# Kernel tuning notes

Hardware: AMD Instinct MI355X
Metric: run time of the kernel (lower is better)

## Reference

```python
import jax, jax.numpy as jnp
import numpy as np

NQ = 200000; K = 4; M = 64; KEY = 64; V = 128; E = 64; B = 512; S = 200

def setup_inputs() -> dict:
    key = jax.random.key(0)
    ks = jax.random.split(key, 16)
    return {
        'q_embed_table': jax.random.normal(ks[0], (NQ + 1, E), jnp.float32) * 0.1,
        'alpha_mean': jax.random.normal(ks[1], (NQ,), jnp.float32) * 0.2,
        'beta_base': jax.random.normal(ks[2], (NQ,), jnp.float32) * 0.5,
        'beta_gaps': jax.random.uniform(ks[3], (NQ, K - 2), jnp.float32) * 0.5 + 0.25,
        'ability_means': jax.random.normal(ks[4], (M, V), jnp.float32) * 0.1,
        'ability_log_vars': jnp.zeros((M, V), jnp.float32),
        'memory_keys': jax.random.normal(ks[5], (M, KEY), jnp.float32),
        'q_to_key_w': jax.random.normal(ks[6], (E, KEY), jnp.float32) / np.sqrt(E),
        'q_to_key_b': jnp.zeros((KEY,), jnp.float32),
        'qa_embed_w': jax.random.normal(ks[7], (2, E), jnp.float32),
        'qa_embed_b': jnp.zeros((E,), jnp.float32),
        'qa_to_ev_w': jax.random.normal(ks[8], (E, V), jnp.float32) / np.sqrt(E),
        'qa_to_ev_b': jnp.zeros((V,), jnp.float32),
        'questions': jax.random.randint(ks[9], (B, S), 0, NQ),
        'responses': jax.random.randint(ks[10], (B, S), 0, K),
    }


def reference(q_embed_table, alpha_mean, beta_base, beta_gaps, ability_means,
              ability_log_vars, memory_keys, q_to_key_w, q_to_key_b,
              qa_embed_w, qa_embed_b, qa_to_ev_w, qa_to_ev_b,
              questions, responses):
    nQ = alpha_mean.shape[0]
    Kc = beta_gaps.shape[1] + 2  # n_categories

    # --- gather question-specific IRT params (irregular gather) ---
    alphas = jnp.exp(alpha_mean[questions])                      # [B,S]
    base = beta_base[questions]                                  # [B,S]
    gaps = jax.nn.softplus(beta_gaps[questions])                 # [B,S,K-2]
    # cumulative thresholds: beta_0 = base, beta_k = beta_{k-1} + gap_{k-1}
    betas = jnp.cumsum(jnp.concatenate([base[..., None], gaps], axis=-1), axis=-1)  # [B,S,K-1]

    # --- attention over memory slots ---
    q_emb = q_embed_table[questions]                             # [B,S,E]
    queries = q_emb @ q_to_key_w + q_to_key_b                    # [B,S,KEY]
    attn = jax.nn.softmax(jnp.einsum('bsk,mk->bsm', queries, memory_keys), axis=-1)  # [B,S,M]

    # --- evidence embedding from (question, response) ---
    qn = questions.astype(jnp.float32) / nQ
    rn = responses.astype(jnp.float32) / (Kc - 1)
    qa = jnp.stack([qn, rn], axis=-1) @ qa_embed_w + qa_embed_b  # [B,S,E]
    evidence = jnp.tanh(qa) @ qa_to_ev_w + qa_to_ev_b            # [B,S,V]

    # --- sequential memory read + per-slot Bayesian scatter update ---
    def step(carry, inp):
        means, log_vars = carry                                  # [M,V] each
        attn_t, ev_t = inp                                       # [B,M], [B,V]
        theta = jnp.mean(attn_t @ means, axis=-1)                # bayesian_read -> [B]
        # precision-weighted update of every slot (evidence_precision = 1)
        w = jnp.mean(attn_t, axis=0)                             # [M] update weights
        ev_mean = jnp.mean(ev_t, axis=0)                         # [V]
        prior_prec = jnp.exp(-log_vars)
        post_prec = prior_prec + w[:, None]
        post_mean = (prior_prec * means + ev_mean[None, :] * w[:, None]) / post_prec
        # torch updates under no_grad -> stop_gradient
        new_means = jax.lax.stop_gradient(post_mean)
        new_lv = jax.lax.stop_gradient(-jnp.log(post_prec))
        return (new_means, new_lv), theta

    (_, _), thetas = jax.lax.scan(
        step, (ability_means, ability_log_vars),
        (attn.transpose(1, 0, 2), evidence.transpose(1, 0, 2)))
    thetas = thetas.T                                            # [B,S]

    # --- GPCM category probabilities ---
    z = alphas[..., None] * (thetas[..., None] - betas)          # [B,S,K-1]
    cum = jnp.concatenate([jnp.zeros_like(z[..., :1]), jnp.cumsum(z, axis=-1)], axis=-1)  # [B,S,K]
    probs = jax.nn.softmax(cum, axis=-1)
    return probs
```

## Files before the change

### kernel.cpp

```cpp
#include <hip/hip_runtime.h>
#include <math.h>

#define M_SLOTS 64
#define E_DIM   64
#define KEY_DIM 64
#define V_DIM   128
#define K_CAT   4
#define S_LEN   200

typedef __attribute__((ext_vector_type(8)))  short short8;
typedef __attribute__((ext_vector_type(16))) float f32x16;

#define OFF_CT     0
#define OFF_BM     2048
#define OFF_WBAR   2112
#define OFF_BBAR   2176
#define OFF_RM0    2240
#define OFF_P0     2304
#define OFF_WSUM   2368
#define OFF_EMSUM  (OFF_WSUM + S_LEN*M_SLOTS)

#define PRE_CT_END   4096
#define PRE_BM_END   4160
#define PRE_WBAR_END 4224
#define PRE_BBAR     4224
#define PRE_RM_BEG   4225
#define PRE_RM_END   4289
#define PRE_Z_BEG    4289
#define PRE_Z_END    (4289 + S_LEN*M_SLOTS + S_LEN)

__device__ __forceinline__ unsigned pk2rne(float lo, float hi) {
    unsigned ul = __float_as_uint(lo); ul += 0x7fffu + ((ul >> 16) & 1u);
    unsigned uh = __float_as_uint(hi); uh += 0x7fffu + ((uh >> 16) & 1u);
    return __builtin_amdgcn_perm(uh, ul, 0x07060302u);
}
__device__ __forceinline__ unsigned short bf16rne(float f) {
    unsigned u = __float_as_uint(f);
    return (unsigned short)((u + 0x7fffu + ((u >> 16) & 1u)) >> 16);
}
__device__ __forceinline__ short8 as_s8(uint4 u) { return __builtin_bit_cast(short8, u); }

__device__ __forceinline__ void gpcm_store(float th, int q,
                                           const float* __restrict__ alpha_mean,
                                           const float* __restrict__ beta_base,
                                           const float* __restrict__ beta_gaps,
                                           float* __restrict__ out, size_t idx) {
    float a  = __expf(alpha_mean[q]);
    float b0 = beta_base[q];
    float2 g = *reinterpret_cast<const float2*>(&beta_gaps[q * (K_CAT - 2)]);
    float g0 = log1pf(__expf(g.x));
    float g1 = log1pf(__expf(g.y));
    float be1 = b0 + g0;
    float be2 = be1 + g1;
    float z0 = a * (th - b0);
    float z1 = a * (th - be1);
    float z2 = a * (th - be2);
    float c1 = z0, c2 = z0 + z1, c3 = z0 + z1 + z2;
    float cm = fmaxf(fmaxf(0.f, c1), fmaxf(c2, c3));
    float e0 = __expf(0.f - cm), e1 = __expf(c1 - cm), e2 = __expf(c2 - cm), e3 = __expf(c3 - cm);
    float si = __fdividef(1.0f, e0 + e1 + e2 + e3);
    float4 o4 = make_float4(e0 * si, e1 * si, e2 * si, e3 * si);
    *reinterpret_cast<float4*>(&out[idx * K_CAT]) = o4;
}

__device__ __forceinline__ void mfma_logits(
    const float* __restrict__ qrow, const unsigned short* __restrict__ ct,
    const float* __restrict__ bm, int h, int p, f32x16 acc[2])
{
    float4 qf[8];
    #pragma unroll
    for (int s = 0; s < 4; ++s) {
        const float4* src = (const float4*)(qrow + s * 16 + h * 8);
        qf[2 * s]     = src[0];
        qf[2 * s + 1] = src[1];
    }
    uint4 af[8];
    #pragma unroll
    for (int mt = 0; mt < 2; ++mt)
        #pragma unroll
        for (int s = 0; s < 4; ++s)
            af[mt * 4 + s] = *(const uint4*)(ct + (p + 32 * mt) * E_DIM + s * 16 + h * 8);
    #pragma unroll
    for (int mt = 0; mt < 2; ++mt)
        #pragma unroll
        for (int g = 0; g < 4; ++g) {
            float4 v = *(const float4*)(bm + 8 * g + 4 * h + 32 * mt);
            acc[mt][4 * g + 0] = v.x; acc[mt][4 * g + 1] = v.y;
            acc[mt][4 * g + 2] = v.z; acc[mt][4 * g + 3] = v.w;
        }
    #pragma unroll
    for (int s = 0; s < 4; ++s) {
        uint4 bf;
        bf.x = pk2rne(qf[2 * s].x,     qf[2 * s].y);
        bf.y = pk2rne(qf[2 * s].z,     qf[2 * s].w);
        bf.z = pk2rne(qf[2 * s + 1].x, qf[2 * s + 1].y);
        bf.w = pk2rne(qf[2 * s + 1].z, qf[2 * s + 1].w);
        short8 bfr = as_s8(bf);
        acc[0] = __builtin_amdgcn_mfma_f32_32x32x16_bf16(as_s8(af[s]),     bfr, acc[0], 0, 0, 0);
        acc[1] = __builtin_amdgcn_mfma_f32_32x32x16_bf16(as_s8(af[4 + s]), bfr, acc[1], 0, 0, 0);
    }
}

__global__ void k_pre(const float* __restrict__ q2k_w, const float* __restrict__ q2k_b,
                      const float* __restrict__ mkeys,
                      const float* __restrict__ ev_w, const float* __restrict__ ev_b,
                      const float* __restrict__ means, const float* __restrict__ logvars,
                      float* __restrict__ ws) {
    int gid = blockIdx.x * blockDim.x + threadIdx.x;
    if (gid < PRE_CT_END) {
        int e = gid >> 6, m = gid & 63;
        float s = 0.f;
        #pragma unroll
        for (int k = 0; k < KEY_DIM; ++k) s = fmaf(q2k_w[e * KEY_DIM + k], mkeys[m * KEY_DIM + k], s);
        ((unsigned short*)ws)[m * E_DIM + e] = bf16rne(s);
    } else if (gid < PRE_BM_END) {
        int m = gid - PRE_CT_END;
        float s = 0.f;
        #pragma unroll
        for (int k = 0; k < KEY_DIM; ++k) s = fmaf(q2k_b[k], mkeys[m * KEY_DIM + k], s);
        ws[OFF_BM + m] = s;
    } else if (gid < PRE_WBAR_END) {
        int e = gid - PRE_BM_END;
        float s = 0.f;
        for (int v = 0; v < V_DIM; ++v) s += ev_w[e * V_DIM + v];
        ws[OFF_WBAR + e] = s * (1.0f / V_DIM);
    } else if (gid == PRE_BBAR) {
        float s = 0.f;
        for (int v = 0; v < V_DIM; ++v) s += ev_b[v];
        ws[OFF_BBAR] = s * (1.0f / V_DIM);
    } else if (gid >= PRE_RM_BEG && gid < PRE_RM_END) {
        int m = gid - PRE_RM_BEG;
        const float4* mr = (const float4*)(means + (size_t)m * V_DIM);
        float s = 0.f;
        #pragma unroll
        for (int i = 0; i < V_DIM / 4; ++i) { float4 v = mr[i]; s += (v.x + v.y) + (v.z + v.w); }
        ws[OFF_RM0 + m] = s * (1.0f / V_DIM);
        ws[OFF_P0 + m]  = __expf(-logvars[(size_t)m * V_DIM]);
    } else if (gid >= PRE_Z_BEG && gid < PRE_Z_END) {
        ws[OFF_WSUM + (gid - PRE_Z_BEG)] = 0.f;
    }
}

__global__ __launch_bounds__(256, 3) void k_attn(
    const float* __restrict__ qtab, const int* __restrict__ qs, const int* __restrict__ rs,
    const float* __restrict__ ws_ro,
    const float* __restrict__ qa_w, const float* __restrict__ qa_b,
    float* __restrict__ wsum, float* __restrict__ emsum,
    int B, float invNQ)
{
    __shared__ float4 lsEv[64];
    const int tid = threadIdx.x, wv = tid >> 6, lane = tid & 63;
    const int h = lane >> 5, p = lane & 31;
    const int t = blockIdx.x;
    const int b = blockIdx.y * 128 + wv * 32 + p;

    const int q = qs[(size_t)b * S_LEN + t];
    const int r = rs[(size_t)b * S_LEN + t];

    if (tid < 64) lsEv[tid] = make_float4(qa_w[tid], qa_w[E_DIM + tid], qa_b[tid],
                                          ws_ro[OFF_WBAR + tid]);
    const float bb = ws_ro[OFF_BBAR];

    f32x16 acc[2];
    mfma_logits(qtab + (size_t)q * E_DIM, (const unsigned short*)ws_ro,
                ws_ro + OFF_BM, h, p, acc);

    float av[32];
    float ssum = 0.f;
    #pragma unroll
    for (int j = 0; j < 16; ++j) { av[j]      = __expf(acc[0][j]); ssum += av[j]; }
    #pragma unroll
    for (int j = 0; j < 16; ++j) { av[16 + j] = __expf(acc[1][j]); ssum += av[16 + j]; }
    ssum += __shfl_xor(ssum, 32);
    const float inv = __fdividef(1.0f, ssum);

    #pragma unroll
    for (int j = 0; j < 32; ++j) av[j] *= inv;
    #pragma unroll
    for (int step = 0; step < 5; ++step) {
        const int sh = 1 << step;
        #pragma unroll
        for (int j = 0; j < (32 >> step) / 2; ++j) {
            float p0 = av[2 * j]     + __shfl_xor(av[2 * j], sh);
            float p1 = av[2 * j + 1] + __shfl_xor(av[2 * j + 1], sh);
            av[j] = (lane & sh) ? p1 : p0;
        }
    }
    {
        const int jj = lane & 31;
        const int m = (jj & 3) + 8 * ((jj >> 2) & 3) + 4 * h + 32 * (jj >> 4);
        atomicAdd(&wsum[t * M_SLOTS + m], av[0]);
    }

    __syncthreads();

    float qn = (float)q * invNQ;
    float rn = (float)r * (1.0f / (K_CAT - 1));
    float evm = 0.f;
    #pragma unroll 8
    for (int e = 0; e < 32; ++e) {
        float4 pv = lsEv[h * 32 + e];
        float qa = fmaf(qn, pv.x, fmaf(rn, pv.y, pv.z));
        float ez = __expf(2.0f * qa);
        evm = fmaf(__fdividef(ez - 1.0f, ez + 1.0f), pv.w, evm);
    }
    evm += __shfl_xor(evm, 32);
    evm += bb;
    #pragma unroll
    for (int o = 16; o; o >>= 1) evm += __shfl_xor(evm, o);
    if (!lane) atomicAdd(&emsum[t], evm);
}

__global__ __launch_bounds__(256, 3) void k_out(
    const float* __restrict__ qtab, const int* __restrict__ qs,
    const float* __restrict__ ws_ro,
    const float* __restrict__ alpha_mean, const float* __restrict__ beta_base,
    const float* __restrict__ beta_gaps, float* __restrict__ out, int B, float invB)
{
    __shared__ float lsW[4][M_SLOTS], lsN[4][M_SLOTS];
    __shared__ float lsRmP[M_SLOTS];
    const int tid = threadIdx.x, wv = tid >> 6, lane = tid & 63;
    const int h = lane >> 5, p = lane & 31;
    const int t = blockIdx.x;
    const int b = blockIdx.y * 128 + wv * 32 + p;

    const int q = qs[(size_t)b * S_LEN + t];

    {
        const float* wsum  = ws_ro + OFF_WSUM;
        const float* emsum = ws_ro + OFF_EMSUM;
        const int seg = (t + 3) >> 2;
        const int s0 = wv * seg, s1 = min(s0 + seg, t);
        float pw = 0.f, pn = 0.f;
        for (int s = s0; s < s1; ++s) {
            float w = wsum[s * M_SLOTS + lane];
            pw += w;
            pn = fmaf(emsum[s], w, pn);
        }
        lsW[wv][lane] = pw; lsN[wv][lane] = pn;
    }
    __syncthreads();
    if (tid < 64) {
        const int m = tid;
        float sw = lsW[0][m] + lsW[1][m] + lsW[2][m] + lsW[3][m];
        float sn = lsN[0][m] + lsN[1][m] + lsN[2][m] + lsN[3][m];
        float den = ws_ro[OFF_P0 + m] + sw * invB;
        float num = ws_ro[OFF_P0 + m] * ws_ro[OFF_RM0 + m] + sn * (invB * invB);
        const int idx = ((m >> 2) & 1) * 32 + ((m >> 5) & 1) * 16 + (m & 3) + 4 * ((m >> 3) & 3);
        lsRmP[idx] = num / den;
    }
    __syncthreads();

    f32x16 acc[2];
    mfma_logits(qtab + (size_t)q * E_DIM, (const unsigned short*)ws_ro,
                ws_ro + OFF_BM, h, p, acc);

    float ssum = 0.f, th = 0.f;
    const float* rmh = lsRmP + h * 32;
    #pragma unroll
    for (int j = 0; j < 16; ++j) {
        float e = __expf(acc[0][j]);
        ssum += e;
        th = fmaf(e, rmh[j], th);
    }
    #pragma unroll
    for (int j = 0; j < 16; ++j) {
        float e = __expf(acc[1][j]);
        ssum += e;
        th = fmaf(e, rmh[16 + j], th);
    }
    ssum += __shfl_xor(ssum, 32);
    th   += __shfl_xor(th, 32);
    th = __fdividef(th, ssum);

    if (!h) gpcm_store(th, q, alpha_mean, beta_base, beta_gaps, out, (size_t)b * S_LEN + t);
}

extern "C" void kernel_launch(void* const* d_in, const int* in_sizes, int n_in,
                              void* d_out, int out_size, void* d_ws, size_t ws_size,
                              hipStream_t stream) {
    const float* qtab       = (const float*)d_in[0];
    const float* alpha_mean = (const float*)d_in[1];
    const float* beta_base  = (const float*)d_in[2];
    const float* beta_gaps  = (const float*)d_in[3];
    const float* ab_means   = (const float*)d_in[4];
    const float* ab_logvars = (const float*)d_in[5];
    const float* mkeys      = (const float*)d_in[6];
    const float* q2k_w      = (const float*)d_in[7];
    const float* q2k_b      = (const float*)d_in[8];
    const float* qa_w       = (const float*)d_in[9];
    const float* qa_b       = (const float*)d_in[10];
    const float* ev_w       = (const float*)d_in[11];
    const float* ev_b       = (const float*)d_in[12];
    const int*   qs         = (const int*)d_in[13];
    const int*   rs         = (const int*)d_in[14];
    float* out = (float*)d_out;
    float* ws  = (float*)d_ws;

    const int NQ = in_sizes[1];
    const int S  = S_LEN;
    const int B  = in_sizes[13] / S;

    float* wsum  = ws + OFF_WSUM;
    float* emsum = ws + OFF_EMSUM;

    k_pre<<<(PRE_Z_END + 255) / 256, 256, 0, stream>>>(
        q2k_w, q2k_b, mkeys, ev_w, ev_b, ab_means, ab_logvars, ws);

    dim3 g(S, B / 128);
    k_attn<<<g, 256, 0, stream>>>(qtab, qs, rs, ws, qa_w, qa_b,
                                  wsum, emsum, B, 1.0f / (float)NQ);

    k_out<<<g, 256, 0, stream>>>(qtab, qs, ws, alpha_mean, beta_base,
                                 beta_gaps, out, B, 1.0f / (float)B);
}
```

Before: 49.37 us.

## Switch attention logits to 16x16x32 bf16 MFMA with 16 rows per wave

Replaces the 32x32x16 MFMA logits tile (32 batch rows per wave, two 32-slot tiles) with 16x16x32 MFMA tiles covering 16 batch rows per wave and four 16-slot tiles. The grid doubles along the batch dimension, the reductions and shuffles are remapped to the new lane layout, and launch bounds go from 3 to 4 waves per SIMD. The goal is smaller accumulators, more resident waves and more blocks for latency hiding. The cost is twice as many blocks, each reloading the shared weight tiles and running more atomics per time step.

After: 56.76 us. +15.0%, slower.

```diff
diff --git a/kernel.cpp b/kernel.cpp
--- a/kernel.cpp
+++ b/kernel.cpp
@@ -8,8 +8,8 @@
 #define K_CAT   4
 #define S_LEN   200
 
-typedef __attribute__((ext_vector_type(8)))  short short8;
-typedef __attribute__((ext_vector_type(16))) float f32x16;
+typedef __attribute__((ext_vector_type(8))) short short8;
+typedef __attribute__((ext_vector_type(4))) float f32x4;
 
 #define OFF_CT     0
 #define OFF_BM     2048
@@ -63,42 +63,37 @@
     *reinterpret_cast<float4*>(&out[idx * K_CAT]) = o4;
 }
 
-__device__ __forceinline__ void mfma_logits(
+__device__ __forceinline__ void mfma_logits16(
     const float* __restrict__ qrow, const unsigned short* __restrict__ ct,
-    const float* __restrict__ bm, int h, int p, f32x16 acc[2])
+    const float* __restrict__ bm, int kg, int p16, f32x4 acc[4])
 {
-    float4 qf[8];
-    #pragma unroll
-    for (int s = 0; s < 4; ++s) {
-        const float4* src = (const float4*)(qrow + s * 16 + h * 8);
-        qf[2 * s]     = src[0];
-        qf[2 * s + 1] = src[1];
-    }
-    uint4 af[8];
-    #pragma unroll
-    for (int mt = 0; mt < 2; ++mt)
-        #pragma unroll
-        for (int s = 0; s < 4; ++s)
-            af[mt * 4 + s] = *(const uint4*)(ct + (p + 32 * mt) * E_DIM + s * 16 + h * 8);
-    #pragma unroll
-    for (int mt = 0; mt < 2; ++mt)
-        #pragma unroll
-        for (int g = 0; g < 4; ++g) {
-            float4 v = *(const float4*)(bm + 8 * g + 4 * h + 32 * mt);
-            acc[mt][4 * g + 0] = v.x; acc[mt][4 * g + 1] = v.y;
-            acc[mt][4 * g + 2] = v.z; acc[mt][4 * g + 3] = v.w;
-        }
-    #pragma unroll
-    for (int s = 0; s < 4; ++s) {
-        uint4 bf;
-        bf.x = pk2rne(qf[2 * s].x,     qf[2 * s].y);
-        bf.y = pk2rne(qf[2 * s].z,     qf[2 * s].w);
-        bf.z = pk2rne(qf[2 * s + 1].x, qf[2 * s + 1].y);
-        bf.w = pk2rne(qf[2 * s + 1].z, qf[2 * s + 1].w);
-        short8 bfr = as_s8(bf);
-        acc[0] = __builtin_amdgcn_mfma_f32_32x32x16_bf16(as_s8(af[s]),     bfr, acc[0], 0, 0, 0);
-        acc[1] = __builtin_amdgcn_mfma_f32_32x32x16_bf16(as_s8(af[4 + s]), bfr, acc[1], 0, 0, 0);
-    }
+    float4 qa = *(const float4*)(qrow + kg * 8);
+    float4 qb = *(const float4*)(qrow + kg * 8 + 4);
+    float4 qc = *(const float4*)(qrow + 32 + kg * 8);
+    float4 qd = *(const float4*)(qrow + 32 + kg * 8 + 4);
+    uint4 af[4][2];
+    #pragma unroll
+    for (int mt = 0; mt < 4; ++mt)
+        #pragma unroll
+        for (int c = 0; c < 2; ++c)
+            af[mt][c] = *(const uint4*)(ct + (mt * 16 + p16) * E_DIM + c * 32 + kg * 8);
+    #pragma unroll
+    for (int mt = 0; mt < 4; ++mt) {
+        float4 v = *(const float4*)(bm + mt * 16 + kg * 4);
+        acc[mt][0] = v.x; acc[mt][1] = v.y; acc[mt][2] = v.z; acc[mt][3] = v.w;
+    }
+    uint4 b0u, b1u;
+    b0u.x = pk2rne(qa.x, qa.y); b0u.y = pk2rne(qa.z, qa.w);
+    b0u.z = pk2rne(qb.x, qb.y); b0u.w = pk2rne(qb.z, qb.w);
+    b1u.x = pk2rne(qc.x, qc.y); b1u.y = pk2rne(qc.z, qc.w);
+    b1u.z = pk2rne(qd.x, qd.y); b1u.w = pk2rne(qd.z, qd.w);
+    short8 b0 = as_s8(b0u), b1 = as_s8(b1u);
+    #pragma unroll
+    for (int mt = 0; mt < 4; ++mt)
+        acc[mt] = __builtin_amdgcn_mfma_f32_16x16x32_bf16(as_s8(af[mt][0]), b0, acc[mt], 0, 0, 0);
+    #pragma unroll
+    for (int mt = 0; mt < 4; ++mt)
+        acc[mt] = __builtin_amdgcn_mfma_f32_16x16x32_bf16(as_s8(af[mt][1]), b1, acc[mt], 0, 0, 0);
 }
 
 __global__ void k_pre(const float* __restrict__ q2k_w, const float* __restrict__ q2k_b,
@@ -141,7 +136,7 @@
     }
 }
 
-__global__ __launch_bounds__(256, 3) void k_attn(
+__global__ __launch_bounds__(256, 4) void k_attn(
     const float* __restrict__ qtab, const int* __restrict__ qs, const int* __restrict__ rs,
     const float* __restrict__ ws_ro,
     const float* __restrict__ qa_w, const float* __restrict__ qa_b,
@@ -150,9 +145,9 @@
 {
     __shared__ float4 lsEv[64];
     const int tid = threadIdx.x, wv = tid >> 6, lane = tid & 63;
-    const int h = lane >> 5, p = lane & 31;
+    const int p16 = lane & 15, kg = lane >> 4;
     const int t = blockIdx.x;
-    const int b = blockIdx.y * 128 + wv * 32 + p;
+    const int b = blockIdx.y * 64 + wv * 16 + p16;
 
     const int q = qs[(size_t)b * S_LEN + t];
     const int r = rs[(size_t)b * S_LEN + t];
@@ -161,34 +156,40 @@
                                           ws_ro[OFF_WBAR + tid]);
     const float bb = ws_ro[OFF_BBAR];
 
-    f32x16 acc[2];
-    mfma_logits(qtab + (size_t)q * E_DIM, (const unsigned short*)ws_ro,
-                ws_ro + OFF_BM, h, p, acc);
-
-    float av[32];
+    f32x4 acc[4];
+    mfma_logits16(qtab + (size_t)q * E_DIM, (const unsigned short*)ws_ro,
+                  ws_ro + OFF_BM, kg, p16, acc);
+
+    float ex[16];
     float ssum = 0.f;
     #pragma unroll
-    for (int j = 0; j < 16; ++j) { av[j]      = __expf(acc[0][j]); ssum += av[j]; }
-    #pragma unroll
-    for (int j = 0; j < 16; ++j) { av[16 + j] = __expf(acc[1][j]); ssum += av[16 + j]; }
+    for (int mt = 0; mt < 4; ++mt)
+        #pragma unroll
+        for (int rg = 0; rg < 4; ++rg) {
+            float e = __expf(acc[mt][rg]);
+            ex[mt * 4 + rg] = e;
+            ssum += e;
+        }
+    ssum += __shfl_xor(ssum, 16);
     ssum += __shfl_xor(ssum, 32);
     const float inv = __fdividef(1.0f, ssum);
 
-    #pragma unroll
-    for (int j = 0; j < 32; ++j) av[j] *= inv;
-    #pragma unroll
-    for (int step = 0; step < 5; ++step) {
+    float av[16];
+    #pragma unroll
+    for (int j = 0; j < 16; ++j) av[j] = ex[j] * inv;
+    #pragma unroll
+    for (int step = 0; step < 4; ++step) {
         const int sh = 1 << step;
         #pragma unroll
-        for (int j = 0; j < (32 >> step) / 2; ++j) {
+        for (int j = 0; j < (16 >> step) / 2; ++j) {
             float p0 = av[2 * j]     + __shfl_xor(av[2 * j], sh);
             float p1 = av[2 * j + 1] + __shfl_xor(av[2 * j + 1], sh);
             av[j] = (lane & sh) ? p1 : p0;
         }
     }
     {
-        const int jj = lane & 31;
-        const int m = (jj & 3) + 8 * ((jj >> 2) & 3) + 4 * h + 32 * (jj >> 4);
+        const int jj = lane & 15;
+        const int m = (jj >> 2) * 16 + kg * 4 + (jj & 3);
         atomicAdd(&wsum[t * M_SLOTS + m], av[0]);
     }
 
@@ -197,32 +198,33 @@
     float qn = (float)q * invNQ;
     float rn = (float)r * (1.0f / (K_CAT - 1));
     float evm = 0.f;
-    #pragma unroll 8
-    for (int e = 0; e < 32; ++e) {
-        float4 pv = lsEv[h * 32 + e];
+    #pragma unroll
+    for (int i = 0; i < 16; ++i) {
+        float4 pv = lsEv[kg * 16 + i];
         float qa = fmaf(qn, pv.x, fmaf(rn, pv.y, pv.z));
         float ez = __expf(2.0f * qa);
         evm = fmaf(__fdividef(ez - 1.0f, ez + 1.0f), pv.w, evm);
     }
+    evm += __shfl_xor(evm, 16);
     evm += __shfl_xor(evm, 32);
     evm += bb;
     #pragma unroll
-    for (int o = 16; o; o >>= 1) evm += __shfl_xor(evm, o);
+    for (int o = 8; o; o >>= 1) evm += __shfl_xor(evm, o);
     if (!lane) atomicAdd(&emsum[t], evm);
 }
 
-__global__ __launch_bounds__(256, 3) void k_out(
+__global__ __launch_bounds__(256, 4) void k_out(
     const float* __restrict__ qtab, const int* __restrict__ qs,
     const float* __restrict__ ws_ro,
     const float* __restrict__ alpha_mean, const float* __restrict__ beta_base,
     const float* __restrict__ beta_gaps, float* __restrict__ out, int B, float invB)
 {
     __shared__ float lsW[4][M_SLOTS], lsN[4][M_SLOTS];
-    __shared__ float lsRmP[M_SLOTS];
+    __shared__ float lsRm[M_SLOTS];
     const int tid = threadIdx.x, wv = tid >> 6, lane = tid & 63;
-    const int h = lane >> 5, p = lane & 31;
+    const int p16 = lane & 15, kg = lane >> 4;
     const int t = blockIdx.x;
-    const int b = blockIdx.y * 128 + wv * 32 + p;
+    const int b = blockIdx.y * 64 + wv * 16 + p16;
 
     const int q = qs[(size_t)b * S_LEN + t];
 
@@ -246,34 +248,30 @@
         float sn = lsN[0][m] + lsN[1][m] + lsN[2][m] + lsN[3][m];
         float den = ws_ro[OFF_P0 + m] + sw * invB;
         float num = ws_ro[OFF_P0 + m] * ws_ro[OFF_RM0 + m] + sn * (invB * invB);
-        const int idx = ((m >> 2) & 1) * 32 + ((m >> 5) & 1) * 16 + (m & 3) + 4 * ((m >> 3) & 3);
-        lsRmP[idx] = num / den;
+        lsRm[m] = num / den;
     }
     __syncthreads();
 
-    f32x16 acc[2];
-    mfma_logits(qtab + (size_t)q * E_DIM, (const unsigned short*)ws_ro,
-                ws_ro + OFF_BM, h, p, acc);
+    f32x4 acc[4];
+    mfma_logits16(qtab + (size_t)q * E_DIM, (const unsigned short*)ws_ro,
+                  ws_ro + OFF_BM, kg, p16, acc);
 
     float ssum = 0.f, th = 0.f;
-    const float* rmh = lsRmP + h * 32;
-    #pragma unroll
-    for (int j = 0; j < 16; ++j) {
-        float e = __expf(acc[0][j]);
-        ssum += e;
-        th = fmaf(e, rmh[j], th);
-    }
-    #pragma unroll
-    for (int j = 0; j < 16; ++j) {
-        float e = __expf(acc[1][j]);
-        ssum += e;
-        th = fmaf(e, rmh[16 + j], th);
-    }
+    #pragma unroll
+    for (int mt = 0; mt < 4; ++mt)
+        #pragma unroll
+        for (int rg = 0; rg < 4; ++rg) {
+            float e = __expf(acc[mt][rg]);
+            ssum += e;
+            th = fmaf(e, lsRm[mt * 16 + kg * 4 + rg], th);
+        }
+    ssum += __shfl_xor(ssum, 16);
     ssum += __shfl_xor(ssum, 32);
+    th   += __shfl_xor(th, 16);
     th   += __shfl_xor(th, 32);
     th = __fdividef(th, ssum);
 
-    if (!h) gpcm_store(th, q, alpha_mean, beta_base, beta_gaps, out, (size_t)b * S_LEN + t);
+    if (kg == 0) gpcm_store(th, q, alpha_mean, beta_base, beta_gaps, out, (size_t)b * S_LEN + t);
 }
 
 extern "C" void kernel_launch(void* const* d_in, const int* in_sizes, int n_in,
@@ -307,7 +305,7 @@
     k_pre<<<(PRE_Z_END + 255) / 256, 256, 0, stream>>>(
         q2k_w, q2k_b, mkeys, ev_w, ev_b, ab_means, ab_logvars, ws);
 
-    dim3 g(S, B / 128);
+    dim3 g(S, B / 64);
     k_attn<<<g, 256, 0, stream>>>(qtab, qs, rs, ws, qa_w, qa_b,
                                   wsum, emsum, B, 1.0f / (float)NQ);
 
```

## Transpose question/response indices and compute per-step ability means in separate kernel

Applied to the files above, without the earlier changes.

k_pre now also transposes the question and response index arrays into time-major order in the workspace, so k_attn and k_out read indices with coalesced accesses instead of strided ones. The prefix-sum reduction of slot weights and evidence, which every k_out block recomputed redundantly, moves into a new k_rm kernel that runs once per time step and writes the posterior means to the workspace. This removes redundant per-block work from k_out but adds one kernel launch and a serial transpose pass over the indices inside k_pre.

Result: slower. 58.98 us (+19.5%).

```diff
diff --git a/kernel.cpp b/kernel.cpp
--- a/kernel.cpp
+++ b/kernel.cpp
@@ -19,6 +19,9 @@
 #define OFF_P0     2304
 #define OFF_WSUM   2368
 #define OFF_EMSUM  (OFF_WSUM + S_LEN*M_SLOTS)
+#define OFF_QST    15424
+#define OFF_RST    (OFF_QST + S_LEN*512)
+#define OFF_RM     (OFF_RST + S_LEN*512)
 
 #define PRE_CT_END   4096
 #define PRE_BM_END   4160
@@ -28,6 +31,7 @@
 #define PRE_RM_END   4289
 #define PRE_Z_BEG    4289
 #define PRE_Z_END    (4289 + S_LEN*M_SLOTS + S_LEN)
+#define PRE_T_BEG    PRE_Z_END
 
 __device__ __forceinline__ unsigned pk2rne(float lo, float hi) {
     unsigned ul = __float_as_uint(lo); ul += 0x7fffu + ((ul >> 16) & 1u);
@@ -105,7 +109,8 @@
                       const float* __restrict__ mkeys,
                       const float* __restrict__ ev_w, const float* __restrict__ ev_b,
                       const float* __restrict__ means, const float* __restrict__ logvars,
-                      float* __restrict__ ws) {
+                      const int* __restrict__ qs, const int* __restrict__ rs,
+                      float* __restrict__ ws, int B) {
     int gid = blockIdx.x * blockDim.x + threadIdx.x;
     if (gid < PRE_CT_END) {
         int e = gid >> 6, m = gid & 63;
@@ -138,12 +143,22 @@
         ws[OFF_P0 + m]  = __expf(-logvars[(size_t)m * V_DIM]);
     } else if (gid >= PRE_Z_BEG && gid < PRE_Z_END) {
         ws[OFF_WSUM + (gid - PRE_Z_BEG)] = 0.f;
+    } else {
+        int i = gid - PRE_T_BEG;
+        const int SB = S_LEN * B;
+        if (i < SB) {
+            int t = i / B, b = i - t * B;
+            ((int*)(ws + OFF_QST))[i] = qs[(size_t)b * S_LEN + t];
+        } else if (i < 2 * SB) {
+            int j = i - SB;
+            int t = j / B, b = j - t * B;
+            ((int*)(ws + OFF_RST))[j] = rs[(size_t)b * S_LEN + t];
+        }
     }
 }
 
 __global__ __launch_bounds__(256, 3) void k_attn(
-    const float* __restrict__ qtab, const int* __restrict__ qs, const int* __restrict__ rs,
-    const float* __restrict__ ws_ro,
+    const float* __restrict__ qtab, const float* __restrict__ ws_ro,
     const float* __restrict__ qa_w, const float* __restrict__ qa_b,
     float* __restrict__ wsum, float* __restrict__ emsum,
     int B, float invNQ)
@@ -154,8 +169,8 @@
     const int t = blockIdx.x;
     const int b = blockIdx.y * 128 + wv * 32 + p;
 
-    const int q = qs[(size_t)b * S_LEN + t];
-    const int r = rs[(size_t)b * S_LEN + t];
+    const int q = ((const int*)(ws_ro + OFF_QST))[t * B + b];
+    const int r = ((const int*)(ws_ro + OFF_RST))[t * B + b];
 
     if (tid < 64) lsEv[tid] = make_float4(qa_w[tid], qa_w[E_DIM + tid], qa_b[tid],
                                           ws_ro[OFF_WBAR + tid]);
@@ -211,44 +226,48 @@
     if (!lane) atomicAdd(&emsum[t], evm);
 }
 
+__global__ __launch_bounds__(64) void k_rm(
+    const float* __restrict__ ws_ro, float* __restrict__ rm, float invB)
+{
+    const int t = blockIdx.x, m = threadIdx.x;
+    const float* wsum  = ws_ro + OFF_WSUM;
+    const float* emsum = ws_ro + OFF_EMSUM;
+    float den = ws_ro[OFF_P0 + m];
+    float num = den * ws_ro[OFF_RM0 + m];
+    int s = 0;
+    for (; s + 4 <= t; s += 4) {
+        float w0 = wsum[(s + 0) * M_SLOTS + m] * invB;
+        float w1 = wsum[(s + 1) * M_SLOTS + m] * invB;
+        float w2 = wsum[(s + 2) * M_SLOTS + m] * invB;
+        float w3 = wsum[(s + 3) * M_SLOTS + m] * invB;
+        num = fmaf(emsum[s + 0] * invB, w0, num); den += w0;
+        num = fmaf(emsum[s + 1] * invB, w1, num); den += w1;
+        num = fmaf(emsum[s + 2] * invB, w2, num); den += w2;
+        num = fmaf(emsum[s + 3] * invB, w3, num); den += w3;
+    }
+    for (; s < t; ++s) {
+        float w = wsum[s * M_SLOTS + m] * invB;
+        num = fmaf(emsum[s] * invB, w, num);
+        den += w;
+    }
+    const int idx = ((m >> 2) & 1) * 32 + ((m >> 5) & 1) * 16 + (m & 3) + 4 * ((m >> 3) & 3);
+    rm[t * M_SLOTS + idx] = num / den;
+}
+
 __global__ __launch_bounds__(256, 3) void k_out(
-    const float* __restrict__ qtab, const int* __restrict__ qs,
-    const float* __restrict__ ws_ro,
+    const float* __restrict__ qtab, const float* __restrict__ ws_ro,
+    const float* __restrict__ rm,
     const float* __restrict__ alpha_mean, const float* __restrict__ beta_base,
-    const float* __restrict__ beta_gaps, float* __restrict__ out, int B, float invB)
+    const float* __restrict__ beta_gaps, float* __restrict__ out, int B)
 {
-    __shared__ float lsW[4][M_SLOTS], lsN[4][M_SLOTS];
-    __shared__ float lsRmP[M_SLOTS];
+    __shared__ float lsRm[M_SLOTS];
     const int tid = threadIdx.x, wv = tid >> 6, lane = tid & 63;
     const int h = lane >> 5, p = lane & 31;
     const int t = blockIdx.x;
     const int b = blockIdx.y * 128 + wv * 32 + p;
 
-    const int q = qs[(size_t)b * S_LEN + t];
-
-    {
-        const float* wsum  = ws_ro + OFF_WSUM;
-        const float* emsum = ws_ro + OFF_EMSUM;
-        const int seg = (t + 3) >> 2;
-        const int s0 = wv * seg, s1 = min(s0 + seg, t);
-        float pw = 0.f, pn = 0.f;
-        for (int s = s0; s < s1; ++s) {
-            float w = wsum[s * M_SLOTS + lane];
-            pw += w;
-            pn = fmaf(emsum[s], w, pn);
-        }
-        lsW[wv][lane] = pw; lsN[wv][lane] = pn;
-    }
-    __syncthreads();
-    if (tid < 64) {
-        const int m = tid;
-        float sw = lsW[0][m] + lsW[1][m] + lsW[2][m] + lsW[3][m];
-        float sn = lsN[0][m] + lsN[1][m] + lsN[2][m] + lsN[3][m];
-        float den = ws_ro[OFF_P0 + m] + sw * invB;
-        float num = ws_ro[OFF_P0 + m] * ws_ro[OFF_RM0 + m] + sn * (invB * invB);
-        const int idx = ((m >> 2) & 1) * 32 + ((m >> 5) & 1) * 16 + (m & 3) + 4 * ((m >> 3) & 3);
-        lsRmP[idx] = num / den;
-    }
+    const int q = ((const int*)(ws_ro + OFF_QST))[t * B + b];
+    if (tid < 64) lsRm[tid] = rm[t * M_SLOTS + tid];
     __syncthreads();
 
     f32x16 acc[2];
@@ -256,7 +275,7 @@
                 ws_ro + OFF_BM, h, p, acc);
 
     float ssum = 0.f, th = 0.f;
-    const float* rmh = lsRmP + h * 32;
+    const float* rmh = lsRm + h * 32;
     #pragma unroll
     for (int j = 0; j < 16; ++j) {
         float e = __expf(acc[0][j]);
@@ -303,14 +322,17 @@
 
     float* wsum  = ws + OFF_WSUM;
     float* emsum = ws + OFF_EMSUM;
-
-    k_pre<<<(PRE_Z_END + 255) / 256, 256, 0, stream>>>(
-        q2k_w, q2k_b, mkeys, ev_w, ev_b, ab_means, ab_logvars, ws);
+    float* rm    = ws + OFF_RM;
+
+    const int pre_items = PRE_T_BEG + 2 * S * B;
+    k_pre<<<(pre_items + 255) / 256, 256, 0, stream>>>(
+        q2k_w, q2k_b, mkeys, ev_w, ev_b, ab_means, ab_logvars, qs, rs, ws, B);
 
     dim3 g(S, B / 128);
-    k_attn<<<g, 256, 0, stream>>>(qtab, qs, rs, ws, qa_w, qa_b,
-                                  wsum, emsum, B, 1.0f / (float)NQ);
-
-    k_out<<<g, 256, 0, stream>>>(qtab, qs, ws, alpha_mean, beta_base,
-                                 beta_gaps, out, B, 1.0f / (float)B);
-}
+    k_attn<<<g, 256, 0, stream>>>(qtab, ws, qa_w, qa_b, wsum, emsum, B, 1.0f / (float)NQ);
+
+    k_rm<<<S, 64, 0, stream>>>(ws, rm, 1.0f / (float)B);
+
+    k_out<<<g, 256, 0, stream>>>(qtab, ws, rm, alpha_mean, beta_base,
+                                 beta_gaps, out, B);
+}
```

## Fuse precompute kernel into attention kernels and replace atomics with per-block partials

Applied to the files above, without the earlier changes.

Removes the k_pre launch. Every block of k_attn and k_out now rebuilds the bf16 key-projection matrix with MFMA into swizzled LDS and computes the bias and mean terms locally. Global atomicAdds into wsum/emsum are replaced by an LDS reduction and plain per-block partial stores, which also removes the need to zero the workspace. k_out sums the four partials. The aim is to save a launch, the zeroing pass and atomic contention, at the cost of redundant per-block recompute and more LDS use.

After: 61.34 us. 24.2% more time.

```diff
diff --git a/kernel.cpp b/kernel.cpp
--- a/kernel.cpp
+++ b/kernel.cpp
@@ -11,23 +11,8 @@
 typedef __attribute__((ext_vector_type(8)))  short short8;
 typedef __attribute__((ext_vector_type(16))) float f32x16;
 
-#define OFF_CT     0
-#define OFF_BM     2048
-#define OFF_WBAR   2112
-#define OFF_BBAR   2176
-#define OFF_RM0    2240
-#define OFF_P0     2304
-#define OFF_WSUM   2368
-#define OFF_EMSUM  (OFF_WSUM + S_LEN*M_SLOTS)
-
-#define PRE_CT_END   4096
-#define PRE_BM_END   4160
-#define PRE_WBAR_END 4224
-#define PRE_BBAR     4224
-#define PRE_RM_BEG   4225
-#define PRE_RM_END   4289
-#define PRE_Z_BEG    4289
-#define PRE_Z_END    (4289 + S_LEN*M_SLOTS + S_LEN)
+#define OFF_WSUMP  0
+#define OFF_EMSUMP (S_LEN * 4 * M_SLOTS)
 
 __device__ __forceinline__ unsigned pk2rne(float lo, float hi) {
     unsigned ul = __float_as_uint(lo); ul += 0x7fffu + ((ul >> 16) & 1u);
@@ -63,31 +48,48 @@
     *reinterpret_cast<float4*>(&out[idx * K_CAT]) = o4;
 }
 
-__device__ __forceinline__ void mfma_logits(
-    const float* __restrict__ qrow, const unsigned short* __restrict__ ct,
-    const float* __restrict__ bm, int h, int p, f32x16 acc[2])
+__device__ __forceinline__ void ct_build(const float* __restrict__ q2k_w,
+                                         const float* __restrict__ mkeys,
+                                         unsigned short* ctL, int wv, int h, int p) {
+    const int m0 = (wv & 1) * 32, e0 = (wv >> 1) * 32;
+    f32x16 d;
+    #pragma unroll
+    for (int i = 0; i < 16; ++i) d[i] = 0.f;
+    #pragma unroll
+    for (int s = 0; s < 4; ++s) {
+        const float* ar = mkeys + (m0 + p) * KEY_DIM + s * 16 + h * 8;
+        const float* br = q2k_w + (e0 + p) * KEY_DIM + s * 16 + h * 8;
+        float4 a0 = *(const float4*)ar, a1 = *(const float4*)(ar + 4);
+        float4 b0 = *(const float4*)br, b1 = *(const float4*)(br + 4);
+        uint4 au, bu;
+        au.x = pk2rne(a0.x, a0.y); au.y = pk2rne(a0.z, a0.w);
+        au.z = pk2rne(a1.x, a1.y); au.w = pk2rne(a1.z, a1.w);
+        bu.x = pk2rne(b0.x, b0.y); bu.y = pk2rne(b0.z, b0.w);
+        bu.z = pk2rne(b1.x, b1.y); bu.w = pk2rne(b1.z, b1.w);
+        d = __builtin_amdgcn_mfma_f32_32x32x16_bf16(as_s8(au), as_s8(bu), d, 0, 0, 0);
+    }
+    #pragma unroll
+    for (int j = 0; j < 16; ++j) {
+        int row = (j & 3) + 8 * ((j >> 2) & 3) + 4 * h;
+        int m = m0 + row, e = e0 + p;
+        int off = m * 128 + (((e * 2)) ^ ((m & 7) << 4));
+        *(unsigned short*)((char*)ctL + off) = bf16rne(d[j]);
+    }
+}
+
+__device__ __forceinline__ void mfma_logits_lds(
+    const float4 qf[8], const unsigned short* ctL, const float* bmL,
+    int h, int p, f32x16 acc[2])
 {
-    float4 qf[8];
-    #pragma unroll
-    for (int s = 0; s < 4; ++s) {
-        const float4* src = (const float4*)(qrow + s * 16 + h * 8);
-        qf[2 * s]     = src[0];
-        qf[2 * s + 1] = src[1];
-    }
-    uint4 af[8];
     #pragma unroll
     for (int mt = 0; mt < 2; ++mt)
         #pragma unroll
-        for (int s = 0; s < 4; ++s)
-            af[mt * 4 + s] = *(const uint4*)(ct + (p + 32 * mt) * E_DIM + s * 16 + h * 8);
-    #pragma unroll
-    for (int mt = 0; mt < 2; ++mt)
-        #pragma unroll
         for (int g = 0; g < 4; ++g) {
-            float4 v = *(const float4*)(bm + 8 * g + 4 * h + 32 * mt);
+            float4 v = *(const float4*)(bmL + 8 * g + 4 * h + 32 * mt);
             acc[mt][4 * g + 0] = v.x; acc[mt][4 * g + 1] = v.y;
             acc[mt][4 * g + 2] = v.z; acc[mt][4 * g + 3] = v.w;
         }
+    const int sw = (p & 7) << 4;
     #pragma unroll
     for (int s = 0; s < 4; ++s) {
         uint4 bf;
@@ -96,74 +98,75 @@
         bf.z = pk2rne(qf[2 * s + 1].x, qf[2 * s + 1].y);
         bf.w = pk2rne(qf[2 * s + 1].z, qf[2 * s + 1].w);
         short8 bfr = as_s8(bf);
-        acc[0] = __builtin_amdgcn_mfma_f32_32x32x16_bf16(as_s8(af[s]),     bfr, acc[0], 0, 0, 0);
-        acc[1] = __builtin_amdgcn_mfma_f32_32x32x16_bf16(as_s8(af[4 + s]), bfr, acc[1], 0, 0, 0);
-    }
-}
-
-__global__ void k_pre(const float* __restrict__ q2k_w, const float* __restrict__ q2k_b,
-                      const float* __restrict__ mkeys,
-                      const float* __restrict__ ev_w, const float* __restrict__ ev_b,
-                      const float* __restrict__ means, const float* __restrict__ logvars,
-                      float* __restrict__ ws) {
-    int gid = blockIdx.x * blockDim.x + threadIdx.x;
-    if (gid < PRE_CT_END) {
-        int e = gid >> 6, m = gid & 63;
-        float s = 0.f;
-        #pragma unroll
-        for (int k = 0; k < KEY_DIM; ++k) s = fmaf(q2k_w[e * KEY_DIM + k], mkeys[m * KEY_DIM + k], s);
-        ((unsigned short*)ws)[m * E_DIM + e] = bf16rne(s);
-    } else if (gid < PRE_BM_END) {
-        int m = gid - PRE_CT_END;
-        float s = 0.f;
-        #pragma unroll
-        for (int k = 0; k < KEY_DIM; ++k) s = fmaf(q2k_b[k], mkeys[m * KEY_DIM + k], s);
-        ws[OFF_BM + m] = s;
-    } else if (gid < PRE_WBAR_END) {
-        int e = gid - PRE_BM_END;
-        float s = 0.f;
-        for (int v = 0; v < V_DIM; ++v) s += ev_w[e * V_DIM + v];
-        ws[OFF_WBAR + e] = s * (1.0f / V_DIM);
-    } else if (gid == PRE_BBAR) {
-        float s = 0.f;
-        for (int v = 0; v < V_DIM; ++v) s += ev_b[v];
-        ws[OFF_BBAR] = s * (1.0f / V_DIM);
-    } else if (gid >= PRE_RM_BEG && gid < PRE_RM_END) {
-        int m = gid - PRE_RM_BEG;
-        const float4* mr = (const float4*)(means + (size_t)m * V_DIM);
-        float s = 0.f;
-        #pragma unroll
-        for (int i = 0; i < V_DIM / 4; ++i) { float4 v = mr[i]; s += (v.x + v.y) + (v.z + v.w); }
-        ws[OFF_RM0 + m] = s * (1.0f / V_DIM);
-        ws[OFF_P0 + m]  = __expf(-logvars[(size_t)m * V_DIM]);
-    } else if (gid >= PRE_Z_BEG && gid < PRE_Z_END) {
-        ws[OFF_WSUM + (gid - PRE_Z_BEG)] = 0.f;
+        const int ebyte = (s * 32 + h * 16) ^ sw;
+        uint4 a0 = *(const uint4*)((const char*)ctL + p * 128 + ebyte);
+        uint4 a1 = *(const uint4*)((const char*)ctL + (p + 32) * 128 + ebyte);
+        acc[0] = __builtin_amdgcn_mfma_f32_32x32x16_bf16(as_s8(a0), bfr, acc[0], 0, 0, 0);
+        acc[1] = __builtin_amdgcn_mfma_f32_32x32x16_bf16(as_s8(a1), bfr, acc[1], 0, 0, 0);
     }
 }
 
 __global__ __launch_bounds__(256, 3) void k_attn(
     const float* __restrict__ qtab, const int* __restrict__ qs, const int* __restrict__ rs,
-    const float* __restrict__ ws_ro,
+    const float* __restrict__ q2k_w, const float* __restrict__ q2k_b,
+    const float* __restrict__ mkeys,
     const float* __restrict__ qa_w, const float* __restrict__ qa_b,
-    float* __restrict__ wsum, float* __restrict__ emsum,
+    const float* __restrict__ ev_w, const float* __restrict__ ev_b,
+    float* __restrict__ wsum_p, float* __restrict__ emsum_p,
     int B, float invNQ)
 {
-    __shared__ float4 lsEv[64];
+    __shared__ unsigned short ctL[M_SLOTS * E_DIM];
+    __shared__ float bmL[M_SLOTS];
+    __shared__ float4 lsEv[E_DIM];
+    __shared__ float lsBB;
+    __shared__ float lsFold[4][M_SLOTS];
+    __shared__ float lsEvw[4];
     const int tid = threadIdx.x, wv = tid >> 6, lane = tid & 63;
     const int h = lane >> 5, p = lane & 31;
-    const int t = blockIdx.x;
-    const int b = blockIdx.y * 128 + wv * 32 + p;
+    const int t = blockIdx.x, by = blockIdx.y;
+    const int b = by * 128 + wv * 32 + p;
 
     const int q = qs[(size_t)b * S_LEN + t];
     const int r = rs[(size_t)b * S_LEN + t];
-
-    if (tid < 64) lsEv[tid] = make_float4(qa_w[tid], qa_w[E_DIM + tid], qa_b[tid],
-                                          ws_ro[OFF_WBAR + tid]);
-    const float bb = ws_ro[OFF_BBAR];
+    const float* qrow = qtab + (size_t)q * E_DIM;
+    float4 qf[8];
+    #pragma unroll
+    for (int s = 0; s < 4; ++s) {
+        const float4* src = (const float4*)(qrow + s * 16 + h * 8);
+        qf[2 * s] = src[0]; qf[2 * s + 1] = src[1];
+    }
+
+    ct_build(q2k_w, mkeys, ctL, wv, h, p);
+    if (wv == 1) {
+        float s = 0.f;
+        const float4* mk = (const float4*)(mkeys + lane * KEY_DIM);
+        const float4* qb = (const float4*)q2k_b;
+        #pragma unroll
+        for (int i = 0; i < KEY_DIM / 4; ++i) {
+            float4 a = mk[i], c = qb[i];
+            s += a.x * c.x + a.y * c.y + a.z * c.z + a.w * c.w;
+        }
+        bmL[lane] = s;
+        float bbv = ev_b[lane] + ev_b[64 + lane];
+        #pragma unroll
+        for (int o = 32; o; o >>= 1) bbv += __shfl_xor(bbv, o);
+        if (!lane) lsBB = bbv * (1.0f / V_DIM);
+    }
+    if (wv == 0) {
+        float wb = 0.f;
+        const float4* er = (const float4*)(ev_w + (size_t)lane * V_DIM);
+        #pragma unroll
+        for (int i = 0; i < V_DIM / 4; ++i) {
+            float4 v = er[i];
+            wb += (v.x + v.y) + (v.z + v.w);
+        }
+        lsEv[lane] = make_float4(qa_w[lane], qa_w[E_DIM + lane], qa_b[lane],
+                                 wb * (1.0f / V_DIM));
+    }
+    __syncthreads();
 
     f32x16 acc[2];
-    mfma_logits(qtab + (size_t)q * E_DIM, (const unsigned short*)ws_ro,
-                ws_ro + OFF_BM, h, p, acc);
+    mfma_logits_lds(qf, ctL, bmL, h, p, acc);
 
     float av[32];
     float ssum = 0.f;
@@ -189,10 +192,8 @@
     {
         const int jj = lane & 31;
         const int m = (jj & 3) + 8 * ((jj >> 2) & 3) + 4 * h + 32 * (jj >> 4);
-        atomicAdd(&wsum[t * M_SLOTS + m], av[0]);
-    }
-
-    __syncthreads();
+        lsFold[wv][m] = av[0];
+    }
 
     float qn = (float)q * invNQ;
     float rn = (float)r * (1.0f / (K_CAT - 1));
@@ -205,55 +206,101 @@
         evm = fmaf(__fdividef(ez - 1.0f, ez + 1.0f), pv.w, evm);
     }
     evm += __shfl_xor(evm, 32);
-    evm += bb;
+    evm += lsBB;
     #pragma unroll
     for (int o = 16; o; o >>= 1) evm += __shfl_xor(evm, o);
-    if (!lane) atomicAdd(&emsum[t], evm);
+    if (!lane) lsEvw[wv] = evm;
+    __syncthreads();
+
+    if (wv == 0) {
+        float s4 = lsFold[0][lane] + lsFold[1][lane] + lsFold[2][lane] + lsFold[3][lane];
+        wsum_p[(size_t)(t * 4 + by) * M_SLOTS + lane] = s4;
+        if (!lane) emsum_p[t * 4 + by] = lsEvw[0] + lsEvw[1] + lsEvw[2] + lsEvw[3];
+    }
 }
 
 __global__ __launch_bounds__(256, 3) void k_out(
     const float* __restrict__ qtab, const int* __restrict__ qs,
-    const float* __restrict__ ws_ro,
+    const float* __restrict__ q2k_w, const float* __restrict__ q2k_b,
+    const float* __restrict__ mkeys,
+    const float* __restrict__ means, const float* __restrict__ logvars,
+    const float* __restrict__ wsum_p, const float* __restrict__ emsum_p,
     const float* __restrict__ alpha_mean, const float* __restrict__ beta_base,
-    const float* __restrict__ beta_gaps, float* __restrict__ out, int B, float invB)
+    const float* __restrict__ beta_gaps, float* __restrict__ out,
+    int B, float invB)
 {
+    __shared__ unsigned short ctL[M_SLOTS * E_DIM];
+    __shared__ float bmL[M_SLOTS];
     __shared__ float lsW[4][M_SLOTS], lsN[4][M_SLOTS];
+    __shared__ float lsRm0[M_SLOTS], lsP0[M_SLOTS];
     __shared__ float lsRmP[M_SLOTS];
     const int tid = threadIdx.x, wv = tid >> 6, lane = tid & 63;
     const int h = lane >> 5, p = lane & 31;
-    const int t = blockIdx.x;
-    const int b = blockIdx.y * 128 + wv * 32 + p;
+    const int t = blockIdx.x, by = blockIdx.y;
+    const int b = by * 128 + wv * 32 + p;
 
     const int q = qs[(size_t)b * S_LEN + t];
+    const float* qrow = qtab + (size_t)q * E_DIM;
+    float4 qf[8];
+    #pragma unroll
+    for (int s = 0; s < 4; ++s) {
+        const float4* src = (const float4*)(qrow + s * 16 + h * 8);
+        qf[2 * s] = src[0]; qf[2 * s + 1] = src[1];
+    }
+
+    ct_build(q2k_w, mkeys, ctL, wv, h, p);
+    if (wv == 1) {
+        float s = 0.f;
+        const float4* mk = (const float4*)(mkeys + lane * KEY_DIM);
+        const float4* qb = (const float4*)q2k_b;
+        #pragma unroll
+        for (int i = 0; i < KEY_DIM / 4; ++i) {
+            float4 a = mk[i], c = qb[i];
+            s += a.x * c.x + a.y * c.y + a.z * c.z + a.w * c.w;
+        }
+        bmL[lane] = s;
+    }
+    if (wv == 2) {
+        float s = 0.f;
+        const float4* mr = (const float4*)(means + (size_t)lane * V_DIM);
+        #pragma unroll
+        for (int i = 0; i < V_DIM / 4; ++i) {
+            float4 v = mr[i];
+            s += (v.x + v.y) + (v.z + v.w);
+        }
+        lsRm0[lane] = s * (1.0f / V_DIM);
+        lsP0[lane]  = __expf(-logvars[(size_t)lane * V_DIM]);
+    }
 
     {
-        const float* wsum  = ws_ro + OFF_WSUM;
-        const float* emsum = ws_ro + OFF_EMSUM;
         const int seg = (t + 3) >> 2;
         const int s0 = wv * seg, s1 = min(s0 + seg, t);
         float pw = 0.f, pn = 0.f;
         for (int s = s0; s < s1; ++s) {
-            float w = wsum[s * M_SLOTS + lane];
+            const float* wp = wsum_p + (size_t)s * 4 * M_SLOTS + lane;
+            float w = wp[0] + wp[M_SLOTS] + wp[2 * M_SLOTS] + wp[3 * M_SLOTS];
+            const float* ep = emsum_p + s * 4;
+            float em = (ep[0] + ep[1]) + (ep[2] + ep[3]);
             pw += w;
-            pn = fmaf(emsum[s], w, pn);
+            pn = fmaf(em, w, pn);
         }
         lsW[wv][lane] = pw; lsN[wv][lane] = pn;
     }
     __syncthreads();
+
     if (tid < 64) {
         const int m = tid;
         float sw = lsW[0][m] + lsW[1][m] + lsW[2][m] + lsW[3][m];
         float sn = lsN[0][m] + lsN[1][m] + lsN[2][m] + lsN[3][m];
-        float den = ws_ro[OFF_P0 + m] + sw * invB;
-        float num = ws_ro[OFF_P0 + m] * ws_ro[OFF_RM0 + m] + sn * (invB * invB);
+        float den = lsP0[m] + sw * invB;
+        float num = fmaf(lsP0[m], lsRm0[m], sn * (invB * invB));
         const int idx = ((m >> 2) & 1) * 32 + ((m >> 5) & 1) * 16 + (m & 3) + 4 * ((m >> 3) & 3);
         lsRmP[idx] = num / den;
     }
     __syncthreads();
 
     f32x16 acc[2];
-    mfma_logits(qtab + (size_t)q * E_DIM, (const unsigned short*)ws_ro,
-                ws_ro + OFF_BM, h, p, acc);
+    mfma_logits_lds(qf, ctL, bmL, h, p, acc);
 
     float ssum = 0.f, th = 0.f;
     const float* rmh = lsRmP + h * 32;
@@ -301,16 +348,16 @@
     const int S  = S_LEN;
     const int B  = in_sizes[13] / S;
 
-    float* wsum  = ws + OFF_WSUM;
-    float* emsum = ws + OFF_EMSUM;
-
-    k_pre<<<(PRE_Z_END + 255) / 256, 256, 0, stream>>>(
-        q2k_w, q2k_b, mkeys, ev_w, ev_b, ab_means, ab_logvars, ws);
+    float* wsum_p  = ws + OFF_WSUMP;
+    float* emsum_p = ws + OFF_EMSUMP;
 
     dim3 g(S, B / 128);
-    k_attn<<<g, 256, 0, stream>>>(qtab, qs, rs, ws, qa_w, qa_b,
-                                  wsum, emsum, B, 1.0f / (float)NQ);
-
-    k_out<<<g, 256, 0, stream>>>(qtab, qs, ws, alpha_mean, beta_base,
-                                 beta_gaps, out, B, 1.0f / (float)B);
-}
+    k_attn<<<g, 256, 0, stream>>>(qtab, qs, rs, q2k_w, q2k_b, mkeys,
+                                  qa_w, qa_b, ev_w, ev_b,
+                                  wsum_p, emsum_p, B, 1.0f / (float)NQ);
+
+    k_out<<<g, 256, 0, stream>>>(qtab, qs, q2k_w, q2k_b, mkeys,
+                                 ab_means, ab_logvars, wsum_p, emsum_p,
+                                 alpha_mean, beta_base, beta_gaps, out,
+                                 B, 1.0f / (float)B);
+}
```
